# Optimization experiments

Measured on AMD Instinct MI355X. Metric: run time of the kernel, lower is better.

## Reference

```python
import jax, jax.numpy as jnp
import numpy as np

DIM = 768
HEADS = 12
HEAD_DIM = DIM // HEADS
SCALE = HEAD_DIM ** -0.5


def setup_inputs() -> dict:
    key = jax.random.key(0)
    k1, k2, k3, k4, k5 = jax.random.split(key, 5)
    x = jax.random.normal(k1, (8, 1024, DIM), dtype=jnp.float32)
    # torch Linear default init ~ U(-1/sqrt(fan_in), 1/sqrt(fan_in)); scale similarly
    s = 1.0 / np.sqrt(DIM)
    qkv_w = jax.random.uniform(k2, (3 * DIM, DIM), minval=-s, maxval=s, dtype=jnp.float32)
    qkv_b = jax.random.uniform(k3, (3 * DIM,), minval=-s, maxval=s, dtype=jnp.float32)
    proj_w = jax.random.uniform(k4, (DIM, DIM), minval=-s, maxval=s, dtype=jnp.float32)
    proj_b = jax.random.uniform(k5, (DIM,), minval=-s, maxval=s, dtype=jnp.float32)
    return {"x": x, "qkv_w": qkv_w, "qkv_b": qkv_b, "proj_w": proj_w, "proj_b": proj_b}


def reference(x, qkv_w, qkv_b, proj_w, proj_b):
    B, N, C = x.shape
    qkv = x @ qkv_w.T + qkv_b                      # [B, N, 3C]
    qkv = qkv.reshape(B, N, 3, HEADS, HEAD_DIM)
    q = jnp.transpose(qkv[:, :, 0], (0, 2, 1, 3))  # [B, H, N, D]
    k = jnp.transpose(qkv[:, :, 1], (0, 2, 1, 3))
    v = jnp.transpose(qkv[:, :, 2], (0, 2, 1, 3))
    attn = jnp.einsum('bhnd,bhmd->bhnm', q, k) * SCALE  # [B, H, N, N]
    attn = jax.nn.softmax(attn, axis=-1)
    out = jnp.einsum('bhnm,bhmd->bhnd', attn, v)   # [B, H, N, D]
    out = jnp.transpose(out, (0, 2, 1, 3)).reshape(B, N, C)
    return out @ proj_w.T + proj_b
```

## Files before the change

### kernel.cpp

```cpp
#include <hip/hip_runtime.h>
#include <stdint.h>

typedef unsigned short ushort_t;
typedef __attribute__((ext_vector_type(8))) short short8;
typedef __attribute__((ext_vector_type(4))) float f32x4;
typedef __attribute__((address_space(1))) uint32_t as1_u32;
typedef __attribute__((address_space(3))) uint32_t as3_u32;

#define MFMA16(a, b, c) __builtin_amdgcn_mfma_f32_16x16x32_bf16(a, b, c, 0, 0, 0)

#define PIPE_BAR3() asm volatile("s_waitcnt vmcnt(3)\n\ts_barrier" ::: "memory")
#define PIPE_BAR0() asm volatile("s_waitcnt vmcnt(0)\n\ts_barrier" ::: "memory")
#define BAR_RAW()   asm volatile("s_barrier" ::: "memory")

__device__ __forceinline__ void cp16(const void* g, void* l) {
    __builtin_amdgcn_global_load_lds((as1_u32*)(uintptr_t)g,
                                     (as3_u32*)(uint32_t)(uintptr_t)l, 16, 0, 0);
}

__device__ __forceinline__ ushort_t f2bf(float f) {
    uint32_t u = __float_as_uint(f);
    u += 0x7fffu + ((u >> 16) & 1u);
    return (ushort_t)(u >> 16);
}

__global__ __launch_bounds__(256) void cvt3_kernel(const float* __restrict__ x,
                                                   const float* __restrict__ w1,
                                                   const float* __restrict__ w2,
                                                   ushort_t* __restrict__ xb,
                                                   ushort_t* __restrict__ wb1,
                                                   ushort_t* __restrict__ wb2) {
    const int bid = blockIdx.x;
    const float4* src;
    ushort4* dst;
    int i;
    if (bid < 6144)      { src = (const float4*)x;  dst = (ushort4*)xb;  i = bid * 256 + threadIdx.x; }
    else if (bid < 7872) { src = (const float4*)w1; dst = (ushort4*)wb1; i = (bid - 6144) * 256 + threadIdx.x; }
    else                 { src = (const float4*)w2; dst = (ushort4*)wb2; i = (bid - 7872) * 256 + threadIdx.x; }
    float4 v = src[i];
    ushort4 o;
    o.x = f2bf(v.x); o.y = f2bf(v.y); o.z = f2bf(v.z); o.w = f2bf(v.w);
    dst[i] = o;
}

__global__ __launch_bounds__(256) void qkv_gemm(const ushort_t* __restrict__ xb,
                                                const ushort_t* __restrict__ wq,
                                                const float* __restrict__ bias,
                                                ushort_t* __restrict__ Qg,
                                                ushort_t* __restrict__ Kg,
                                                ushort_t* __restrict__ Vt) {
    __shared__ __align__(16) ushort_t smem[12288];
    const int t = threadIdx.x, w = t >> 6, lane = t & 63;
    const int m16 = lane & 15, q = lane >> 4;
    const int wgid = blockIdx.x;
    const int xcd = wgid & 7, idx = wgid >> 3;
    const int n0 = (idx % 36) * 64;
    const int m0 = (xcd * 8 + idx / 36) * 128;
    ushort_t* const A0 = smem;
    ushort_t* const B0 = smem + 4096;
    ushort_t* const A1 = smem + 6144;
    ushort_t* const B1 = smem + 10240;

    f32x4 acc[2][4];
#pragma unroll
    for (int i = 0; i < 2; ++i)
#pragma unroll
        for (int j = 0; j < 4; ++j) acc[i][j] = (f32x4)0.f;

    auto issueT = [&](int kk, ushort_t* As, ushort_t* Bs) {
#pragma unroll
        for (int s = 0; s < 2; ++s) {
            const int c = s * 256 + t;
            cp16(&xb[(m0 + (c >> 2)) * 768 + kk + (c & 3) * 8], &As[(s * 256 + w * 64) * 8]);
        }
        cp16(&wq[(n0 + (t >> 2)) * 768 + kk + (t & 3) * 8], &Bs[(w * 64) * 8]);
    };

    issueT(0, A0, B0);
    issueT(32, A1, B1);
#pragma unroll 2
    for (int kki = 0; kki < 24; ++kki) {
        if (kki < 23) { PIPE_BAR3(); } else { PIPE_BAR0(); }
        ushort_t* As = (kki & 1) ? A1 : A0;
        ushort_t* Bs = (kki & 1) ? B1 : B0;
        short8 a[2], b[4];
#pragma unroll
        for (int i = 0; i < 2; ++i) a[i] = *(const short8*)&As[(w * 32 + i * 16 + m16) * 32 + q * 8];
#pragma unroll
        for (int j = 0; j < 4; ++j) b[j] = *(const short8*)&Bs[(j * 16 + m16) * 32 + q * 8];
#pragma unroll
        for (int i = 0; i < 2; ++i)
#pragma unroll
            for (int j = 0; j < 4; ++j) acc[i][j] = MFMA16(a[i], b[j], acc[i][j]);
        BAR_RAW();
        if (kki < 22) issueT((kki + 2) * 32, As, Bs);
    }

    const int three = n0 / 768;
    const int b_idx = m0 >> 10;
    const int col0 = n0 - three * 768;
    const int hh = col0 >> 6;

    if (three < 2) {
        ushort_t* dst = three ? Kg : Qg;
        const float scale = three ? 1.0f : 0.18033688011112042f;
#pragma unroll
        for (int j = 0; j < 4; ++j) {
            float bj = bias[n0 + j * 16 + m16];
#pragma unroll
            for (int i = 0; i < 2; ++i)
#pragma unroll
                for (int r = 0; r < 4; ++r)
                    smem[(w * 32 + i * 16 + q * 4 + r) * 72 + j * 16 + m16] =
                        f2bf((acc[i][j][r] + bj) * scale);
        }
        __syncthreads();
#pragma unroll
        for (int u4 = 0; u4 < 4; ++u4) {
            int u = u4 * 256 + t;
            int row = u >> 3, cg = u & 7;
            uint4 vv = *(const uint4*)&smem[row * 72 + cg * 8];
            int n = (m0 & 1023) + row;
            *(uint4*)&dst[((b_idx * 12 + hh) * 1024 + n) * 64 + cg * 8] = vv;
        }
    } else {
        const int nq_base = (m0 & 1023) + w * 32;
#pragma unroll
        for (int j = 0; j < 4; ++j) {
            int dd = j * 16 + m16;
            float bj = bias[1536 + col0 + dd];
            ushort_t* base = Vt + ((b_idx * 12 + hh) * 64 + dd) * 1024;
#pragma unroll
            for (int i = 0; i < 2; ++i) {
                ushort4 pk;
                pk.x = f2bf(acc[i][j][0] + bj);
                pk.y = f2bf(acc[i][j][1] + bj);
                pk.z = f2bf(acc[i][j][2] + bj);
                pk.w = f2bf(acc[i][j][3] + bj);
                *(ushort4*)&base[nq_base + i * 16 + q * 4] = pk;
            }
        }
    }
}

__global__ __launch_bounds__(256) void attn_kernel(const ushort_t* __restrict__ Qg,
                                                   const ushort_t* __restrict__ Kg,
                                                   const ushort_t* __restrict__ Vt,
                                                   ushort_t* __restrict__ Og) {
    __shared__ __align__(16) ushort_t Ks[64 * 64];
    __shared__ __align__(16) ushort_t Vs[64 * 64];
    __shared__ __align__(16) ushort_t Ps[4 * 16 * 72];
    const int t = threadIdx.x, w = t >> 6, lane = t & 63;
    const int m16 = lane & 15, q = lane >> 4;
    const int wgid = blockIdx.x;
    const int xcd = wgid & 7, idx = wgid >> 3;
    const int bh = xcd * 12 + (idx >> 4);
    const int qt = idx & 15;
    const int b = bh / 12, h = bh % 12;
    const ushort_t* Qbh = Qg + bh * 65536;
    const ushort_t* Kbh = Kg + bh * 65536;
    const ushort_t* Vbh = Vt + bh * 65536;
    ushort_t* Pw = &Ps[w * 1152];

    const int q0 = qt * 64 + w * 16;
    short8 qf[2];
#pragma unroll
    for (int kd = 0; kd < 2; ++kd)
        qf[kd] = *(const short8*)&Qbh[(q0 + m16) * 64 + kd * 32 + q * 8];

    f32x4 o[4];
#pragma unroll
    for (int ds = 0; ds < 4; ++ds) o[ds] = (f32x4)0.f;
    float l_run = 0.f;

    for (int kt = 0; kt < 16; ++kt) {
        const int key0 = kt * 64;
#pragma unroll
        for (int p = 0; p < 2; ++p) {
            const int c = p * 256 + t;
            const int lbase = (p * 256 + w * 64) * 8;
            { int key = c >> 3, g = c & 7;
              cp16(&Kbh[(key0 + key) * 64 + ((g ^ (key & 7)) * 8)], &Ks[lbase]); }
            { int d = c >> 3, g2 = c & 7;
              cp16(&Vbh[d * 1024 + key0 + ((g2 ^ (d & 7)) * 8)], &Vs[lbase]); }
        }
        __syncthreads();

        f32x4 st[4];
#pragma unroll
        for (int ks = 0; ks < 4; ++ks) {
            const ushort_t* kr = &Ks[(ks * 16 + m16) * 64];
            short8 a0 = *(const short8*)&kr[(q ^ (m16 & 7)) * 8];
            short8 a1 = *(const short8*)&kr[((4 + q) ^ (m16 & 7)) * 8];
            st[ks] = MFMA16(a1, qf[1], MFMA16(a0, qf[0], (f32x4)0.f));
        }

        float ps = 0.f;
#pragma unroll
        for (int ks = 0; ks < 4; ++ks) {
            float p0 = exp2f(st[ks][0]);
            float p1 = exp2f(st[ks][1]);
            float p2 = exp2f(st[ks][2]);
            float p3 = exp2f(st[ks][3]);
            ps += (p0 + p1) + (p2 + p3);
            uint32_t u0 = __float_as_uint(p0) + 0x8000u;
            uint32_t u1 = __float_as_uint(p1) + 0x8000u;
            uint32_t u2 = __float_as_uint(p2) + 0x8000u;
            uint32_t u3 = __float_as_uint(p3) + 0x8000u;
            uint2 pk;
            pk.x = __builtin_amdgcn_perm(u1, u0, 0x07060302u);
            pk.y = __builtin_amdgcn_perm(u3, u2, 0x07060302u);
            *(uint2*)&Pw[m16 * 72 + ks * 16 + q * 4] = pk;
        }
        ps += __shfl_xor(ps, 16, 64);
        ps += __shfl_xor(ps, 32, 64);
        l_run += ps;
#pragma unroll
        for (int kkk = 0; kkk < 2; ++kkk) {
            short8 ap = *(const short8*)&Pw[m16 * 72 + kkk * 32 + q * 8];
#pragma unroll
            for (int ds = 0; ds < 4; ++ds) {
                short8 vb = *(const short8*)&Vs[(ds * 16 + m16) * 64 + (((kkk * 4 + q) ^ (m16 & 7)) * 8)];
                o[ds] = MFMA16(ap, vb, o[ds]);
            }
        }
        __syncthreads();
    }
    {
        float linv = 1.f / l_run;
#pragma unroll
        for (int r = 0; r < 4; ++r) {
            float lr = __shfl(linv, q * 4 + r, 64);
            int row = b * 1024 + q0 + q * 4 + r;
#pragma unroll
            for (int ds = 0; ds < 4; ++ds)
                Og[row * 768 + h * 64 + ds * 16 + m16] = f2bf(o[ds][r] * lr);
        }
    }
}

__global__ __launch_bounds__(256) void proj_gemm(const ushort_t* __restrict__ Ob,
                                                 const ushort_t* __restrict__ wp,
                                                 const float* __restrict__ bias,
                                                 float* __restrict__ out) {
    __shared__ __align__(16) ushort_t smem[12288];
    const int t = threadIdx.x, w = t >> 6, lane = t & 63;
    const int m16 = lane & 15, q = lane >> 4;
    const int wgid = blockIdx.x;
    const int xcd = wgid & 7, idx = wgid >> 3;
    const int n0 = (idx % 12) * 64;
    const int m0 = (xcd * 8 + idx / 12) * 128;
    ushort_t* const A0 = smem;
    ushort_t* const B0 = smem + 4096;
    ushort_t* const A1 = smem + 6144;
    ushort_t* const B1 = smem + 10240;

    f32x4 acc[2][4];
#pragma unroll
    for (int i = 0; i < 2; ++i)
#pragma unroll
        for (int j = 0; j < 4; ++j) acc[i][j] = (f32x4)0.f;

    auto issueT = [&](int kk, ushort_t* As, ushort_t* Bs) {
#pragma unroll
        for (int s = 0; s < 2; ++s) {
            const int c = s * 256 + t;
            cp16(&Ob[(m0 + (c >> 2)) * 768 + kk + (c & 3) * 8], &As[(s * 256 + w * 64) * 8]);
        }
        cp16(&wp[(n0 + (t >> 2)) * 768 + kk + (t & 3) * 8], &Bs[(w * 64) * 8]);
    };

    issueT(0, A0, B0);
    issueT(32, A1, B1);
#pragma unroll 2
    for (int kki = 0; kki < 24; ++kki) {
        if (kki < 23) { PIPE_BAR3(); } else { PIPE_BAR0(); }
        ushort_t* As = (kki & 1) ? A1 : A0;
        ushort_t* Bs = (kki & 1) ? B1 : B0;
        short8 a[2], b[4];
#pragma unroll
        for (int i = 0; i < 2; ++i) a[i] = *(const short8*)&As[(w * 32 + i * 16 + m16) * 32 + q * 8];
#pragma unroll
        for (int j = 0; j < 4; ++j) b[j] = *(const short8*)&Bs[(j * 16 + m16) * 32 + q * 8];
#pragma unroll
        for (int i = 0; i < 2; ++i)
#pragma unroll
            for (int j = 0; j < 4; ++j) acc[i][j] = MFMA16(a[i], b[j], acc[i][j]);
        BAR_RAW();
        if (kki < 22) issueT((kki + 2) * 32, As, Bs);
    }

#pragma unroll
    for (int j = 0; j < 4; ++j) {
        int col = n0 + j * 16 + m16;
        float bj = bias[col];
#pragma unroll
        for (int i = 0; i < 2; ++i)
#pragma unroll
            for (int r = 0; r < 4; ++r) {
                int row = m0 + w * 32 + i * 16 + q * 4 + r;
                out[row * 768 + col] = acc[i][j][r] + bj;
            }
    }
}

extern "C" void kernel_launch(void* const* d_in, const int* in_sizes, int n_in,
                              void* d_out, int out_size, void* d_ws, size_t ws_size,
                              hipStream_t stream) {
    const float* x      = (const float*)d_in[0];
    const float* qkv_w  = (const float*)d_in[1];
    const float* qkv_b  = (const float*)d_in[2];
    const float* proj_w = (const float*)d_in[3];
    const float* proj_b = (const float*)d_in[4];
    float* out = (float*)d_out;

    char* ws = (char*)d_ws;
    ushort_t* xb    = (ushort_t*)(ws);
    ushort_t* wqkv  = (ushort_t*)(ws + 12582912);
    ushort_t* wproj = (ushort_t*)(ws + 16121856);
    ushort_t* Qg    = (ushort_t*)(ws + 17301504);
    ushort_t* Kg    = (ushort_t*)(ws + 29884416);
    ushort_t* Vt    = (ushort_t*)(ws + 42467328);
    ushort_t* Og    = (ushort_t*)(ws + 55050240);

    cvt3_kernel<<<8448, 256, 0, stream>>>(x, qkv_w, proj_w, xb, wqkv, wproj);
    qkv_gemm<<<2304, 256, 0, stream>>>(xb, wqkv, qkv_b, Qg, Kg, Vt);
    attn_kernel<<<1536, 256, 0, stream>>>(Qg, Kg, Vt, Og);
    proj_gemm<<<768, 256, 0, stream>>>(Og, wproj, proj_b, out);
}
```

Baseline: 208.6 us.

## Pre-pack GEMM operands into MFMA fragment layout and load directly from global

The conversion kernel and the attention output now write bf16 data in a tiled 16x32 fragment-major layout, so each lane's MFMA operand is one contiguous 16-byte global load. Both GEMMs drop the LDS double-buffered staging and barriers and read fragments straight from global memory through the cache. This removes LDS traffic and barrier stalls, but gives up explicit prefetch pipelining and relies on L2/L1 reuse across waves for the shared B tiles. The attention epilogue now does scattered 2-byte stores into the packed layout.

```diff
diff --git a/kernel.cpp b/kernel.cpp
--- a/kernel.cpp
+++ b/kernel.cpp
@@ -9,10 +9,6 @@
 
 #define MFMA16(a, b, c) __builtin_amdgcn_mfma_f32_16x16x32_bf16(a, b, c, 0, 0, 0)
 
-#define PIPE_BAR3() asm volatile("s_waitcnt vmcnt(3)\n\ts_barrier" ::: "memory")
-#define PIPE_BAR0() asm volatile("s_waitcnt vmcnt(0)\n\ts_barrier" ::: "memory")
-#define BAR_RAW()   asm volatile("s_barrier" ::: "memory")
-
 __device__ __forceinline__ void cp16(const void* g, void* l) {
     __builtin_amdgcn_global_load_lds((as1_u32*)(uintptr_t)g,
                                      (as3_u32*)(uint32_t)(uintptr_t)l, 16, 0, 0);
@@ -23,6 +19,7 @@
     u += 0x7fffu + ((u >> 16) & 1u);
     return (ushort_t)(u >> 16);
 }
+
 
 __global__ __launch_bounds__(256) void cvt3_kernel(const float* __restrict__ x,
                                                    const float* __restrict__ w1,
@@ -32,34 +29,38 @@
                                                    ushort_t* __restrict__ wb2) {
     const int bid = blockIdx.x;
     const float4* src;
-    ushort4* dst;
+    ushort_t* dst;
     int i;
-    if (bid < 6144)      { src = (const float4*)x;  dst = (ushort4*)xb;  i = bid * 256 + threadIdx.x; }
-    else if (bid < 7872) { src = (const float4*)w1; dst = (ushort4*)wb1; i = (bid - 6144) * 256 + threadIdx.x; }
-    else                 { src = (const float4*)w2; dst = (ushort4*)wb2; i = (bid - 7872) * 256 + threadIdx.x; }
+    if (bid < 6144)      { src = (const float4*)x;  dst = xb;  i = bid * 256 + threadIdx.x; }
+    else if (bid < 7872) { src = (const float4*)w1; dst = wb1; i = (bid - 6144) * 256 + threadIdx.x; }
+    else                 { src = (const float4*)w2; dst = wb2; i = (bid - 7872) * 256 + threadIdx.x; }
     float4 v = src[i];
     ushort4 o;
     o.x = f2bf(v.x); o.y = f2bf(v.y); o.z = f2bf(v.z); o.w = f2bf(v.w);
-    dst[i] = o;
-}
-
-__global__ __launch_bounds__(256) void qkv_gemm(const ushort_t* __restrict__ xb,
-                                                const ushort_t* __restrict__ wq,
+    const int e0 = i * 4;
+    const int r = e0 / 768, k0 = e0 - r * 768;
+    const int off = (((r >> 4) * 24 + (k0 >> 5)) << 9) +
+                    (((r & 15) + (((k0 & 31) >> 3) << 4)) << 3) + (k0 & 7);
+    *(ushort4*)&dst[off] = o;
+}
+
+__global__ __launch_bounds__(256) void qkv_gemm(const ushort_t* __restrict__ xp,
+                                                const ushort_t* __restrict__ wqp,
                                                 const float* __restrict__ bias,
                                                 ushort_t* __restrict__ Qg,
                                                 ushort_t* __restrict__ Kg,
                                                 ushort_t* __restrict__ Vt) {
-    __shared__ __align__(16) ushort_t smem[12288];
+    __shared__ __align__(16) ushort_t smem[9216];
     const int t = threadIdx.x, w = t >> 6, lane = t & 63;
     const int m16 = lane & 15, q = lane >> 4;
     const int wgid = blockIdx.x;
     const int xcd = wgid & 7, idx = wgid >> 3;
     const int n0 = (idx % 36) * 64;
     const int m0 = (xcd * 8 + idx / 36) * 128;
-    ushort_t* const A0 = smem;
-    ushort_t* const B0 = smem + 4096;
-    ushort_t* const A1 = smem + 6144;
-    ushort_t* const B1 = smem + 10240;
+
+    const int rA = (m0 >> 4) + w * 2;
+    const int rB = n0 >> 4;
+    const int le = lane << 3;
 
     f32x4 acc[2][4];
 #pragma unroll
@@ -67,33 +68,19 @@
 #pragma unroll
         for (int j = 0; j < 4; ++j) acc[i][j] = (f32x4)0.f;
 
-    auto issueT = [&](int kk, ushort_t* As, ushort_t* Bs) {
-#pragma unroll
-        for (int s = 0; s < 2; ++s) {
-            const int c = s * 256 + t;
-            cp16(&xb[(m0 + (c >> 2)) * 768 + kk + (c & 3) * 8], &As[(s * 256 + w * 64) * 8]);
-        }
-        cp16(&wq[(n0 + (t >> 2)) * 768 + kk + (t & 3) * 8], &Bs[(w * 64) * 8]);
-    };
-
-    issueT(0, A0, B0);
-    issueT(32, A1, B1);
-#pragma unroll 2
+#pragma unroll 4
     for (int kki = 0; kki < 24; ++kki) {
-        if (kki < 23) { PIPE_BAR3(); } else { PIPE_BAR0(); }
-        ushort_t* As = (kki & 1) ? A1 : A0;
-        ushort_t* Bs = (kki & 1) ? B1 : B0;
         short8 a[2], b[4];
 #pragma unroll
-        for (int i = 0; i < 2; ++i) a[i] = *(const short8*)&As[(w * 32 + i * 16 + m16) * 32 + q * 8];
-#pragma unroll
-        for (int j = 0; j < 4; ++j) b[j] = *(const short8*)&Bs[(j * 16 + m16) * 32 + q * 8];
+        for (int i = 0; i < 2; ++i)
+            a[i] = *(const short8*)&xp[(((rA + i) * 24 + kki) << 9) + le];
+#pragma unroll
+        for (int j = 0; j < 4; ++j)
+            b[j] = *(const short8*)&wqp[(((rB + j) * 24 + kki) << 9) + le];
 #pragma unroll
         for (int i = 0; i < 2; ++i)
 #pragma unroll
             for (int j = 0; j < 4; ++j) acc[i][j] = MFMA16(a[i], b[j], acc[i][j]);
-        BAR_RAW();
-        if (kki < 22) issueT((kki + 2) * 32, As, Bs);
     }
 
     const int three = n0 / 768;
@@ -146,7 +133,7 @@
 __global__ __launch_bounds__(256) void attn_kernel(const ushort_t* __restrict__ Qg,
                                                    const ushort_t* __restrict__ Kg,
                                                    const ushort_t* __restrict__ Vt,
-                                                   ushort_t* __restrict__ Og) {
+                                                   ushort_t* __restrict__ Ogp) {
     __shared__ __align__(16) ushort_t Ks[64 * 64];
     __shared__ __align__(16) ushort_t Vs[64 * 64];
     __shared__ __align__(16) ushort_t Ps[4 * 16 * 72];
@@ -227,33 +214,35 @@
         __syncthreads();
     }
     {
+        const int rt = (b * 64 + qt * 4 + w) * 24 + h * 2;
         float linv = 1.f / l_run;
 #pragma unroll
         for (int r = 0; r < 4; ++r) {
             float lr = __shfl(linv, q * 4 + r, 64);
-            int row = b * 1024 + q0 + q * 4 + r;
-#pragma unroll
-            for (int ds = 0; ds < 4; ++ds)
-                Og[row * 768 + h * 64 + ds * 16 + m16] = f2bf(o[ds][r] * lr);
-        }
-    }
-}
-
-__global__ __launch_bounds__(256) void proj_gemm(const ushort_t* __restrict__ Ob,
-                                                 const ushort_t* __restrict__ wp,
+#pragma unroll
+            for (int ds = 0; ds < 4; ++ds) {
+                int off = ((rt + (ds >> 1)) << 9) +
+                          ((q * 4 + r + (((ds & 1) << 1) + (m16 >> 3)) * 16) << 3) + (m16 & 7);
+                Ogp[off] = f2bf(o[ds][r] * lr);
+            }
+        }
+    }
+}
+
+__global__ __launch_bounds__(256) void proj_gemm(const ushort_t* __restrict__ Ogp,
+                                                 const ushort_t* __restrict__ wpp,
                                                  const float* __restrict__ bias,
                                                  float* __restrict__ out) {
-    __shared__ __align__(16) ushort_t smem[12288];
     const int t = threadIdx.x, w = t >> 6, lane = t & 63;
     const int m16 = lane & 15, q = lane >> 4;
     const int wgid = blockIdx.x;
     const int xcd = wgid & 7, idx = wgid >> 3;
     const int n0 = (idx % 12) * 64;
     const int m0 = (xcd * 8 + idx / 12) * 128;
-    ushort_t* const A0 = smem;
-    ushort_t* const B0 = smem + 4096;
-    ushort_t* const A1 = smem + 6144;
-    ushort_t* const B1 = smem + 10240;
+
+    const int rA = (m0 >> 4) + w * 2;
+    const int rB = n0 >> 4;
+    const int le = lane << 3;
 
     f32x4 acc[2][4];
 #pragma unroll
@@ -261,33 +250,19 @@
 #pragma unroll
         for (int j = 0; j < 4; ++j) acc[i][j] = (f32x4)0.f;
 
-    auto issueT = [&](int kk, ushort_t* As, ushort_t* Bs) {
-#pragma unroll
-        for (int s = 0; s < 2; ++s) {
-            const int c = s * 256 + t;
-            cp16(&Ob[(m0 + (c >> 2)) * 768 + kk + (c & 3) * 8], &As[(s * 256 + w * 64) * 8]);
-        }
-        cp16(&wp[(n0 + (t >> 2)) * 768 + kk + (t & 3) * 8], &Bs[(w * 64) * 8]);
-    };
-
-    issueT(0, A0, B0);
-    issueT(32, A1, B1);
-#pragma unroll 2
+#pragma unroll 4
     for (int kki = 0; kki < 24; ++kki) {
-        if (kki < 23) { PIPE_BAR3(); } else { PIPE_BAR0(); }
-        ushort_t* As = (kki & 1) ? A1 : A0;
-        ushort_t* Bs = (kki & 1) ? B1 : B0;
         short8 a[2], b[4];
 #pragma unroll
-        for (int i = 0; i < 2; ++i) a[i] = *(const short8*)&As[(w * 32 + i * 16 + m16) * 32 + q * 8];
-#pragma unroll
-        for (int j = 0; j < 4; ++j) b[j] = *(const short8*)&Bs[(j * 16 + m16) * 32 + q * 8];
+        for (int i = 0; i < 2; ++i)
+            a[i] = *(const short8*)&Ogp[(((rA + i) * 24 + kki) << 9) + le];
+#pragma unroll
+        for (int j = 0; j < 4; ++j)
+            b[j] = *(const short8*)&wpp[(((rB + j) * 24 + kki) << 9) + le];
 #pragma unroll
         for (int i = 0; i < 2; ++i)
 #pragma unroll
             for (int j = 0; j < 4; ++j) acc[i][j] = MFMA16(a[i], b[j], acc[i][j]);
-        BAR_RAW();
-        if (kki < 22) issueT((kki + 2) * 32, As, Bs);
     }
 
 #pragma unroll
```

Measured after the change: 208.8 us. No clear change (+0.1%).

## Pre-pack x and QKV weights into MFMA tile layout and widen proj wave tiles

Applied to the files above, without the earlier changes.

The conversion kernel now writes x and the QKV weight in a tiled layout matching the 16x32 MFMA operand fragments. This lets qkv_gemm load A and B fragments straight from global memory with no LDS staging or barriers. Separately, proj_gemm drops to 128 threads per block, with each wave computing a 64x64 tile and the wait count adjusted to the extra loads. The risk is that qkv_gemm loses its software pipelining and LDS reuse and now depends on the cache to absorb global loads that are issued repeatedly.

```diff
diff --git a/kernel.cpp b/kernel.cpp
--- a/kernel.cpp
+++ b/kernel.cpp
@@ -9,7 +9,7 @@
 
 #define MFMA16(a, b, c) __builtin_amdgcn_mfma_f32_16x16x32_bf16(a, b, c, 0, 0, 0)
 
-#define PIPE_BAR3() asm volatile("s_waitcnt vmcnt(3)\n\ts_barrier" ::: "memory")
+#define PIPE_BAR6() asm volatile("s_waitcnt vmcnt(6)\n\ts_barrier" ::: "memory")
 #define PIPE_BAR0() asm volatile("s_waitcnt vmcnt(0)\n\ts_barrier" ::: "memory")
 #define BAR_RAW()   asm volatile("s_barrier" ::: "memory")
 
@@ -23,6 +23,7 @@
     u += 0x7fffu + ((u >> 16) & 1u);
     return (ushort_t)(u >> 16);
 }
+
 
 __global__ __launch_bounds__(256) void cvt3_kernel(const float* __restrict__ x,
                                                    const float* __restrict__ w1,
@@ -30,36 +31,48 @@
                                                    ushort_t* __restrict__ xb,
                                                    ushort_t* __restrict__ wb1,
                                                    ushort_t* __restrict__ wb2) {
-    const int bid = blockIdx.x;
-    const float4* src;
-    ushort4* dst;
-    int i;
-    if (bid < 6144)      { src = (const float4*)x;  dst = (ushort4*)xb;  i = bid * 256 + threadIdx.x; }
-    else if (bid < 7872) { src = (const float4*)w1; dst = (ushort4*)wb1; i = (bid - 6144) * 256 + threadIdx.x; }
-    else                 { src = (const float4*)w2; dst = (ushort4*)wb2; i = (bid - 7872) * 256 + threadIdx.x; }
-    float4 v = src[i];
-    ushort4 o;
-    o.x = f2bf(v.x); o.y = f2bf(v.y); o.z = f2bf(v.z); o.w = f2bf(v.w);
-    dst[i] = o;
-}
-
-__global__ __launch_bounds__(256) void qkv_gemm(const ushort_t* __restrict__ xb,
-                                                const ushort_t* __restrict__ wq,
+    int c = blockIdx.x * 256 + threadIdx.x;
+    if (c < 1007616) {
+        const float* src;
+        ushort_t* dst;
+        if (c < 786432) { src = x;  dst = xb; }
+        else            { src = w1; dst = wb1; c -= 786432; }
+        const int tile = c >> 6, inner = c & 63;
+        const int rt = tile / 24, kt = tile - rt * 24;
+        const int r = rt * 16 + (inner & 15);
+        const int k = kt * 32 + ((inner >> 4) << 3);
+        const float4* s4 = (const float4*)&src[r * 768 + k];
+        float4 v0 = s4[0], v1 = s4[1];
+        ushort_t o[8];
+        o[0] = f2bf(v0.x); o[1] = f2bf(v0.y); o[2] = f2bf(v0.z); o[3] = f2bf(v0.w);
+        o[4] = f2bf(v1.x); o[5] = f2bf(v1.y); o[6] = f2bf(v1.z); o[7] = f2bf(v1.w);
+        *(uint4*)&dst[c << 3] = *(const uint4*)o;
+    } else {
+        int i = c - 1007616;
+        float4 v = ((const float4*)w2)[i];
+        ushort4 o;
+        o.x = f2bf(v.x); o.y = f2bf(v.y); o.z = f2bf(v.z); o.w = f2bf(v.w);
+        ((ushort4*)wb2)[i] = o;
+    }
+}
+
+__global__ __launch_bounds__(256) void qkv_gemm(const ushort_t* __restrict__ xp,
+                                                const ushort_t* __restrict__ wqp,
                                                 const float* __restrict__ bias,
                                                 ushort_t* __restrict__ Qg,
                                                 ushort_t* __restrict__ Kg,
                                                 ushort_t* __restrict__ Vt) {
-    __shared__ __align__(16) ushort_t smem[12288];
+    __shared__ __align__(16) ushort_t smem[9216];
     const int t = threadIdx.x, w = t >> 6, lane = t & 63;
     const int m16 = lane & 15, q = lane >> 4;
     const int wgid = blockIdx.x;
     const int xcd = wgid & 7, idx = wgid >> 3;
     const int n0 = (idx % 36) * 64;
     const int m0 = (xcd * 8 + idx / 36) * 128;
-    ushort_t* const A0 = smem;
-    ushort_t* const B0 = smem + 4096;
-    ushort_t* const A1 = smem + 6144;
-    ushort_t* const B1 = smem + 10240;
+
+    const int rA = (m0 >> 4) + w * 2;
+    const int rB = n0 >> 4;
+    const int le = lane << 3;
 
     f32x4 acc[2][4];
 #pragma unroll
@@ -67,33 +80,19 @@
 #pragma unroll
         for (int j = 0; j < 4; ++j) acc[i][j] = (f32x4)0.f;
 
-    auto issueT = [&](int kk, ushort_t* As, ushort_t* Bs) {
-#pragma unroll
-        for (int s = 0; s < 2; ++s) {
-            const int c = s * 256 + t;
-            cp16(&xb[(m0 + (c >> 2)) * 768 + kk + (c & 3) * 8], &As[(s * 256 + w * 64) * 8]);
-        }
-        cp16(&wq[(n0 + (t >> 2)) * 768 + kk + (t & 3) * 8], &Bs[(w * 64) * 8]);
-    };
-
-    issueT(0, A0, B0);
-    issueT(32, A1, B1);
-#pragma unroll 2
+#pragma unroll 4
     for (int kki = 0; kki < 24; ++kki) {
-        if (kki < 23) { PIPE_BAR3(); } else { PIPE_BAR0(); }
-        ushort_t* As = (kki & 1) ? A1 : A0;
-        ushort_t* Bs = (kki & 1) ? B1 : B0;
         short8 a[2], b[4];
 #pragma unroll
-        for (int i = 0; i < 2; ++i) a[i] = *(const short8*)&As[(w * 32 + i * 16 + m16) * 32 + q * 8];
-#pragma unroll
-        for (int j = 0; j < 4; ++j) b[j] = *(const short8*)&Bs[(j * 16 + m16) * 32 + q * 8];
-#pragma unroll
         for (int i = 0; i < 2; ++i)
+            a[i] = *(const short8*)&xp[(((rA + i) * 24 + kki) << 9) + le];
+#pragma unroll
+        for (int j = 0; j < 4; ++j)
+            b[j] = *(const short8*)&wqp[(((rB + j) * 24 + kki) << 9) + le];
+#pragma unroll
+        for (int i = 0; i < 2; ++i)
 #pragma unroll
             for (int j = 0; j < 4; ++j) acc[i][j] = MFMA16(a[i], b[j], acc[i][j]);
-        BAR_RAW();
-        if (kki < 22) issueT((kki + 2) * 32, As, Bs);
     }
 
     const int three = n0 / 768;
@@ -239,7 +238,7 @@
     }
 }
 
-__global__ __launch_bounds__(256) void proj_gemm(const ushort_t* __restrict__ Ob,
+__global__ __launch_bounds__(128) void proj_gemm(const ushort_t* __restrict__ Ob,
                                                  const ushort_t* __restrict__ wp,
                                                  const float* __restrict__ bias,
                                                  float* __restrict__ out) {
@@ -255,35 +254,39 @@
     ushort_t* const A1 = smem + 6144;
     ushort_t* const B1 = smem + 10240;
 
-    f32x4 acc[2][4];
-#pragma unroll
-    for (int i = 0; i < 2; ++i)
+    f32x4 acc[4][4];
+#pragma unroll
+    for (int i = 0; i < 4; ++i)
 #pragma unroll
         for (int j = 0; j < 4; ++j) acc[i][j] = (f32x4)0.f;
 
     auto issueT = [&](int kk, ushort_t* As, ushort_t* Bs) {
 #pragma unroll
+        for (int s = 0; s < 4; ++s) {
+            const int c = s * 128 + t;
+            cp16(&Ob[(m0 + (c >> 2)) * 768 + kk + (c & 3) * 8], &As[(s * 128 + w * 64) * 8]);
+        }
+#pragma unroll
         for (int s = 0; s < 2; ++s) {
-            const int c = s * 256 + t;
-            cp16(&Ob[(m0 + (c >> 2)) * 768 + kk + (c & 3) * 8], &As[(s * 256 + w * 64) * 8]);
-        }
-        cp16(&wp[(n0 + (t >> 2)) * 768 + kk + (t & 3) * 8], &Bs[(w * 64) * 8]);
+            const int c = s * 128 + t;
+            cp16(&wp[(n0 + (c >> 2)) * 768 + kk + (c & 3) * 8], &Bs[(s * 128 + w * 64) * 8]);
+        }
     };
 
     issueT(0, A0, B0);
     issueT(32, A1, B1);
 #pragma unroll 2
     for (int kki = 0; kki < 24; ++kki) {
-        if (kki < 23) { PIPE_BAR3(); } else { PIPE_BAR0(); }
+        if (kki < 23) { PIPE_BAR6(); } else { PIPE_BAR0(); }
         ushort_t* As = (kki & 1) ? A1 : A0;
         ushort_t* Bs = (kki & 1) ? B1 : B0;
-        short8 a[2], b[4];
-#pragma unroll
-        for (int i = 0; i < 2; ++i) a[i] = *(const short8*)&As[(w * 32 + i * 16 + m16) * 32 + q * 8];
+        short8 a[4], b[4];
+#pragma unroll
+        for (int i = 0; i < 4; ++i) a[i] = *(const short8*)&As[(w * 64 + i * 16 + m16) * 32 + q * 8];
 #pragma unroll
         for (int j = 0; j < 4; ++j) b[j] = *(const short8*)&Bs[(j * 16 + m16) * 32 + q * 8];
 #pragma unroll
-        for (int i = 0; i < 2; ++i)
+        for (int i = 0; i < 4; ++i)
 #pragma unroll
             for (int j = 0; j < 4; ++j) acc[i][j] = MFMA16(a[i], b[j], acc[i][j]);
         BAR_RAW();
@@ -295,10 +298,10 @@
         int col = n0 + j * 16 + m16;
         float bj = bias[col];
 #pragma unroll
-        for (int i = 0; i < 2; ++i)
+        for (int i = 0; i < 4; ++i)
 #pragma unroll
             for (int r = 0; r < 4; ++r) {
-                int row = m0 + w * 32 + i * 16 + q * 4 + r;
+                int row = m0 + w * 64 + i * 16 + q * 4 + r;
                 out[row * 768 + col] = acc[i][j][r] + bj;
             }
     }
@@ -323,8 +326,8 @@
     ushort_t* Vt    = (ushort_t*)(ws + 42467328);
     ushort_t* Og    = (ushort_t*)(ws + 55050240);
 
-    cvt3_kernel<<<8448, 256, 0, stream>>>(x, qkv_w, proj_w, xb, wqkv, wproj);
+    cvt3_kernel<<<4512, 256, 0, stream>>>(x, qkv_w, proj_w, xb, wqkv, wproj);
     qkv_gemm<<<2304, 256, 0, stream>>>(xb, wqkv, qkv_b, Qg, Kg, Vt);
     attn_kernel<<<1536, 256, 0, stream>>>(Qg, Kg, Vt, Og);
-    proj_gemm<<<768, 256, 0, stream>>>(Og, wproj, proj_b, out);
-}
+    proj_gemm<<<768, 128, 0, stream>>>(Og, wproj, proj_b, out);
+}
```

Result: faster. 202.6 us (-2.8%).
